# Kernel tuning notes

Measured on AMD Instinct MI355X. Metric: run time of the kernel, lower is better.

Reference implementation:

```python
import jax, jax.numpy as jnp
import numpy as np

T, N, D, V = 512, 256, 1024, 128000  # total tokens, sampled tokens, d_model, vocab


def setup_inputs() -> dict:
    key = jax.random.key(0)
    k1, k2, k3, k4, k5 = jax.random.split(key, 5)
    hidden_states = jax.random.normal(k1, (T, D), dtype=jnp.float32)
    embedding = jax.random.normal(k2, (V, D), dtype=jnp.float32) * 0.02
    # temperatures in [0.5, 1.5): realistic, avoids divide blow-up (0.0 maps to 1.0 in source)
    temperatures = 0.5 + jax.random.uniform(k3, (N,), dtype=jnp.float32)
    # top_p in [0.5, 1.0)
    top_ps = 0.5 + 0.5 * jax.random.uniform(k4, (N,), dtype=jnp.float32)
    last_token_indices = jnp.sort(jax.random.randint(k5, (N,), 0, T))
    return {
        "hidden_states": hidden_states,
        "embedding": embedding,
        "temperatures": temperatures,
        "top_ps": top_ps,
        "last_token_indices": last_token_indices,
    }


def reference(hidden_states, embedding, temperatures, top_ps, last_token_indices):
    # gather last-token hidden states, project to vocab logits
    h = hidden_states[last_token_indices]              # [N, D]
    logits = jnp.einsum("nd,vd->nv", h, embedding)     # [N, V]
    # temperature softmax
    probs = jax.nn.softmax(logits / temperatures[:, None], axis=-1)
    # top-p: descending sort, cumsum, mask tail, renormalize, un-sort
    order = jnp.argsort(-probs, axis=-1)               # descending order indices
    probs_sort = jnp.take_along_axis(probs, order, axis=-1)
    cum = jnp.cumsum(probs_sort, axis=-1)
    mask = (cum - probs_sort) > top_ps[:, None]
    probs_sort = jnp.where(mask, 0.0, probs_sort)
    probs_sort = probs_sort / jnp.sum(probs_sort, axis=-1, keepdims=True)
    inv = jnp.argsort(order, axis=-1)                  # inverse permutation
    probs_f = jnp.take_along_axis(probs_sort, inv, axis=-1)
    # multinomial sampling (one token per row), fixed key for determinism
    tokens = jax.random.categorical(jax.random.key(42), jnp.log(probs_f + 1e-20), axis=-1)
    return probs_f, tokens
```

## Files before the change

kernel.cpp:

```cpp
#include <hip/hip_runtime.h>
#include <stdint.h>

#define N_TOK 256
#define D_MODEL 1024
#define VOCAB 128000
#define NV_ELEMS (256LL * 128000LL)
#define LIST_CAP 24576
#define GLIST_CAP 16384

typedef unsigned long long u64;
typedef uint32_t u32;
typedef __attribute__((ext_vector_type(8))) short bfrag;
typedef __attribute__((ext_vector_type(4))) float facc;

__device__ __forceinline__ uint32_t bf16_rne_bits(float x) {
    uint32_t u = __float_as_uint(x);
    return (u + 0x7fffu + ((u >> 16) & 1u)) >> 16;
}

__device__ __forceinline__ uint32_t rotl32(uint32_t x, int d) {
    return (x << d) | (x >> (32 - d));
}

__device__ __forceinline__ u32 mono32(u32 b) {
    return (b & 0x80000000u) ? ~b : (b | 0x80000000u);
}
__device__ __forceinline__ float unmono32(u32 k) {
    u32 b = (k & 0x80000000u) ? (k & 0x7FFFFFFFu) : ~k;
    return __uint_as_float(b);
}

__device__ __forceinline__ u64 fixmass(float rv) {
    return (u64)(rv * 1073741824.0f);
}

__device__ __forceinline__ uint2 tf_0_42(uint32_t c0, uint32_t c1) {
    const uint32_t ks0 = 0u, ks1 = 42u, ks2 = 0x1BD11BDAu ^ 42u;
    uint32_t x0 = c0 + ks0, x1 = c1 + ks1;
#define R4(a,b,c,d) \
    x0 += x1; x1 = rotl32(x1,a); x1 ^= x0; \
    x0 += x1; x1 = rotl32(x1,b); x1 ^= x0; \
    x0 += x1; x1 = rotl32(x1,c); x1 ^= x0; \
    x0 += x1; x1 = rotl32(x1,d); x1 ^= x0;
    R4(13,15,26,6)   x0 += ks1; x1 += ks2 + 1u;
    R4(17,29,16,24)  x0 += ks2; x1 += ks0 + 2u;
    R4(13,15,26,6)   x0 += ks0; x1 += ks1 + 3u;
    R4(17,29,16,24)  x0 += ks1; x1 += ks2 + 4u;
    R4(13,15,26,6)   x0 += ks2; x1 += ks0 + 5u;
#undef R4
    return make_uint2(x0, x1);
}

__device__ __forceinline__ uint32_t jax_bits(uint32_t j) {
    uint2 r = tf_0_42(0u, j);
    return r.x ^ r.y;
}

__device__ __forceinline__ float jax_gumbel(uint32_t bits) {
    const float TINY = 1.17549435e-38f;
    float u = __uint_as_float((bits >> 9) | 0x3f800000u) - 1.0f;
    u = u + TINY;
    u = fmaxf(TINY, u);
    return -__logf(-__logf(u));
}

__device__ __forceinline__ float rv_of(float l, float rinv) {
    return __expf(l * rinv);
}

__device__ __forceinline__ void async_copy16(const void* g, void* lbase, int lane) {
#if defined(__has_builtin) && __has_builtin(__builtin_amdgcn_global_load_lds)
    __builtin_amdgcn_global_load_lds((const uint32_t*)g, (uint32_t*)lbase, 16, 0, 0);
#else
    *(bfrag*)((char*)lbase + lane * 16) = *(const bfrag*)g;
#endif
}

__device__ __forceinline__ void scan_desc_u64(const u64* h, int nb, u64 carry, u64 P,
                                              int* outCb, u64* outSa) {
    int lane = (int)threadIdx.x & 63;
    int chunk = nb >> 6;
    int top = nb - 1 - lane * chunk;
    u64 ls = 0ull;
    for (int j = 0; j < chunk; ++j) ls += h[top - j];
    u64 incl = ls;
    for (int o = 1; o < 64; o <<= 1) {
        u64 v = __shfl_up(incl, o, 64);
        if (lane >= o) incl += v;
    }
    u64 s0 = carry + incl - ls;
    unsigned long long mask = __ballot(s0 + ls > P);
    if (mask == 0ull) {
        if (lane == 0) { *outCb = 0; *outSa = carry; }
    } else {
        int cstar = (int)__builtin_ctzll(mask);
        if (lane == cstar) {
            u64 sa = s0; int cb = 0;
            for (int j = 0; j < chunk; ++j) {
                int b = top - j;
                if (sa + h[b] > P) { cb = b; break; }
                sa += h[b];
            }
            *outCb = cb; *outSa = sa;
        }
    }
}

__global__ __launch_bounds__(256) void prep_a(
        const float* __restrict__ hidden, const int* __restrict__ idx,
        ushort* __restrict__ wsA) {
    const int m = blockIdx.x;
    const int t = threadIdx.x;
    const float* src = hidden + (long long)idx[m] * D_MODEL;
    const uint32_t swz = (uint32_t)((m & 7) << 4);
    for (int j = 0; j < 4; ++j) {
        int k = t * 4 + j;
        float x = src[k];
        uint32_t hb = bf16_rne_bits(x);
        float hf = __uint_as_float(hb << 16);
        uint32_t lb = bf16_rne_bits(x - hf);
        int kt = k >> 5, kk = k & 31, g = kk >> 3, e = kk & 7;
        char* img = (char*)wsA + (size_t)kt * 32768;
        uint32_t base = (uint32_t)(m * 128 + g * 32);
        *(ushort*)(img + ((base + 0) ^ swz) + e * 2) = (ushort)hb;
        *(ushort*)(img + ((base + 16) ^ swz) + e * 2) = (ushort)lb;
    }
}

__global__ __launch_bounds__(256) void gemm_mfma(
        const ushort* __restrict__ wsA, const float* __restrict__ emb,
        float* __restrict__ logits) {
    __shared__ __align__(16) ushort Aimg[16384];
    __shared__ __align__(16) ushort Bimg[4096];
    const int tid = (int)threadIdx.x;
    const int w = tid >> 6, l = tid & 63;
    const int lr = l & 15, lg = l >> 4;
    const int v0 = blockIdx.x * 64;
    char* Ab = (char*)Aimg;
    char* Bb = (char*)Bimg;

    facc acc[4][4] = {};

    const int rb = tid >> 2, g = tid & 3;
    const float* bbase = emb + (size_t)(v0 + rb) * D_MODEL + g * 8;
    float4 q0 = *(const float4*)(bbase);
    float4 q1 = *(const float4*)(bbase + 4);

    for (int kt = 0; kt < 32; ++kt) {
        __syncthreads();
        const char* asrc = (const char*)wsA + (size_t)kt * 32768;
#pragma unroll
        for (int i = 0; i < 8; ++i) {
            int off = w * 8192 + i * 1024;
            async_copy16(asrc + off + l * 16, Ab + off, l);
        }
        float4 n0 = q0, n1 = q1;
        if (kt < 31) {
            n0 = *(const float4*)(bbase + (kt + 1) * 32);
            n1 = *(const float4*)(bbase + (kt + 1) * 32 + 4);
        }
        {
            float xs[8] = {q0.x, q0.y, q0.z, q0.w, q1.x, q1.y, q1.z, q1.w};
            bfrag h, lo;
#pragma unroll
            for (int e = 0; e < 8; ++e) {
                uint32_t hb = bf16_rne_bits(xs[e]);
                float hf = __uint_as_float(hb << 16);
                uint32_t lb = bf16_rne_bits(xs[e] - hf);
                h[e] = (short)hb; lo[e] = (short)lb;
            }
            uint32_t swz = (uint32_t)((rb & 7) << 4);
            uint32_t base = (uint32_t)(rb * 128 + g * 32);
            *(bfrag*)(Bb + ((base + 0) ^ swz)) = h;
            *(bfrag*)(Bb + ((base + 16) ^ swz)) = lo;
        }
        __syncthreads();
        bfrag bh[4], bl[4];
#pragma unroll
        for (int nj = 0; nj < 4; ++nj) {
            int rbf = nj * 16 + lr;
            uint32_t swz = (uint32_t)((rbf & 7) << 4);
            uint32_t base = (uint32_t)(rbf * 128 + lg * 32);
            bh[nj] = *(const bfrag*)(Bb + ((base + 0) ^ swz));
            bl[nj] = *(const bfrag*)(Bb + ((base + 16) ^ swz));
        }
#pragma unroll
        for (int mi = 0; mi < 4; ++mi) {
            int r = w * 64 + mi * 16 + lr;
            uint32_t swz = (uint32_t)((r & 7) << 4);
            uint32_t base = (uint32_t)(r * 128 + lg * 32);
            bfrag ah = *(const bfrag*)(Ab + ((base + 0) ^ swz));
            bfrag al = *(const bfrag*)(Ab + ((base + 16) ^ swz));
#pragma unroll
            for (int nj = 0; nj < 4; ++nj) {
                acc[mi][nj] = __builtin_amdgcn_mfma_f32_16x16x32_bf16(ah, bh[nj], acc[mi][nj], 0, 0, 0);
                acc[mi][nj] = __builtin_amdgcn_mfma_f32_16x16x32_bf16(ah, bl[nj], acc[mi][nj], 0, 0, 0);
                acc[mi][nj] = __builtin_amdgcn_mfma_f32_16x16x32_bf16(al, bh[nj], acc[mi][nj], 0, 0, 0);
            }
        }
        q0 = n0; q1 = n1;
    }
#pragma unroll
    for (int mi = 0; mi < 4; ++mi) {
        int mbase = w * 64 + mi * 16 + lg * 4;
#pragma unroll
        for (int nj = 0; nj < 4; ++nj) {
            int v = v0 + nj * 16 + lr;
#pragma unroll
            for (int reg = 0; reg < 4; ++reg)
                logits[(size_t)(mbase + reg) * VOCAB + v] = acc[mi][nj][reg];
        }
    }
}

__global__ __launch_bounds__(256) void gemm_kernel(
        const float* __restrict__ hidden, const int* __restrict__ idx,
        const float* __restrict__ emb, float* __restrict__ logits) {
    __shared__ float As[16][64];
    __shared__ float Bs[16][64];
    const int n0 = blockIdx.x * 64, v0 = blockIdx.y * 64;
    const int tid = threadIdx.x;
    const int tx = tid & 15, ty = tid >> 4;
    const int lr = tid >> 2, lk = (tid & 3) * 4;
    float acc[4][4] = {};
    const long long aRow = (long long)idx[n0 + lr] * D_MODEL + lk;
    const long long bRow = (long long)(v0 + lr) * D_MODEL + lk;
    for (int k0 = 0; k0 < D_MODEL; k0 += 16) {
        float4 av = *(const float4*)(hidden + aRow + k0);
        float4 bv = *(const float4*)(emb + bRow + k0);
        __syncthreads();
        As[lk + 0][lr] = av.x; As[lk + 1][lr] = av.y; As[lk + 2][lr] = av.z; As[lk + 3][lr] = av.w;
        Bs[lk + 0][lr] = bv.x; Bs[lk + 1][lr] = bv.y; Bs[lk + 2][lr] = bv.z; Bs[lk + 3][lr] = bv.w;
        __syncthreads();
#pragma unroll
        for (int kk = 0; kk < 16; ++kk) {
            float4 a = *(const float4*)&As[kk][ty * 4];
            float4 b = *(const float4*)&Bs[kk][tx * 4];
            float aa[4] = {a.x, a.y, a.z, a.w};
            float bb[4] = {b.x, b.y, b.z, b.w};
#pragma unroll
            for (int i = 0; i < 4; ++i)
#pragma unroll
                for (int j = 0; j < 4; ++j)
                    acc[i][j] += aa[i] * bb[j];
        }
    }
#pragma unroll
    for (int i = 0; i < 4; ++i) {
        float4 o = make_float4(acc[i][0], acc[i][1], acc[i][2], acc[i][3]);
        *(float4*)(logits + (long long)(n0 + ty * 4 + i) * VOCAB + (v0 + tx * 4)) = o;
    }
}

__global__ __launch_bounds__(512) void hist1_kernel(
        const float* __restrict__ probs, const float* __restrict__ temps,
        u64* __restrict__ ghist) {
    const int row = blockIdx.y, hb = blockIdx.x, tid = (int)threadIdx.x;
    __shared__ u64 h[4096];
    for (int i = tid; i < 4096; i += 512) h[i] = 0ull;
    __syncthreads();
    const float rinv = 1.0f / temps[row];
    const float4* R4 = (const float4*)(probs + (size_t)row * VOCAB);
    const int base4 = hb * 8000;
    for (int i = 0; i < 16; ++i) {
        int j = tid + i * 512;
        if (j < 8000) {
            float4 x = R4[base4 + j];
            float xs[4] = {x.x, x.y, x.z, x.w};
#pragma unroll
            for (int c = 0; c < 4; ++c) {
                u32 key = mono32(__float_as_uint(xs[c]));
                atomicAdd(&h[key >> 20], fixmass(rv_of(xs[c], rinv)));
            }
        }
    }
    __syncthreads();
    u64* gh = ghist + (size_t)row * 4096;
    for (int i = tid; i < 4096; i += 512)
        if (h[i]) atomicAdd(&gh[i], h[i]);
}

__global__ __launch_bounds__(64) void scan1_kernel(
        const u64* __restrict__ ghist, const float* __restrict__ topps,
        u64* __restrict__ rsP, u64* __restrict__ rsCarry, u32* __restrict__ rsCb) {
    const int row = blockIdx.x, lane = (int)threadIdx.x;
    const u64* h = ghist + (size_t)row * 4096;
    u64 S = 0ull;
    for (int j = lane; j < 4096; j += 64) S += h[j];
    for (int o = 32; o >= 1; o >>= 1) S += __shfl_xor(S, o, 64);
    const u64 P = (u64)((double)topps[row] * (double)S);
    __shared__ int sCb; __shared__ u64 sSa;
    scan_desc_u64(h, 4096, 0ull, P, &sCb, &sSa);
    __syncthreads();
    if (lane == 0) { rsP[row] = P; rsCarry[row] = sSa; rsCb[row] = (u32)sCb; }
}

__global__ __launch_bounds__(512) void compact_kernel(
        const float* __restrict__ probs, const u32* __restrict__ rsCb,
        u64* __restrict__ list, u32* __restrict__ listCnt) {
    const int row = blockIdx.y, hb = blockIdx.x, tid = (int)threadIdx.x;
    __shared__ u64 buf[4096];
    __shared__ u32 lcnt, gbase;
    const u32 cb1 = rsCb[row];
    const float4* R4 = (const float4*)(probs + (size_t)row * VOCAB);
    u64* lst = list + (size_t)row * GLIST_CAP;
    const int base4 = hb * 8000;
    if (tid == 0) lcnt = 0u;
    __syncthreads();
    for (int pair = 0; pair < 8; ++pair) {
#pragma unroll
        for (int s = 0; s < 2; ++s) {
            int j = tid + (pair * 2 + s) * 512;
            if (j < 8000) {
                float4 x = R4[base4 + j];
                float xs[4] = {x.x, x.y, x.z, x.w};
#pragma unroll
                for (int c = 0; c < 4; ++c) {
                    u32 key = mono32(__float_as_uint(xs[c]));
                    if ((key >> 20) == cb1) {
                        u32 pos = atomicAdd(&lcnt, 1u);
                        buf[pos] = ((u64)key << 32) | (u32)((base4 + j) * 4 + c);
                    }
                }
            }
        }
        __syncthreads();
        u32 n = lcnt;
        if (n) {
            if (tid == 0) gbase = atomicAdd(&listCnt[row], n);
            __syncthreads();
            u32 gb = gbase;
            for (u32 i2 = tid; i2 < n; i2 += 512) {
                u32 gpos = gb + i2;
                if (gpos < GLIST_CAP) lst[gpos] = buf[i2];
            }
        }
        __syncthreads();
        if (tid == 0) lcnt = 0u;
        __syncthreads();
    }
}

__global__ __launch_bounds__(1024) void resolve_kernel(
        const u64* __restrict__ list, const u32* __restrict__ listCnt,
        const u64* __restrict__ rsP, const u64* __restrict__ rsCarry,
        const u32* __restrict__ rsCb, const float* __restrict__ temps,
        u32* __restrict__ scTs, u32* __restrict__ scTieN,
        float* __restrict__ scInvSp, u32* __restrict__ tieKept) {
    const int row = blockIdx.x, tid = (int)threadIdx.x;
    __shared__ u64 h2[1024];
    __shared__ u32 c3[1024];
    __shared__ int sCb; __shared__ u64 sSa;
    __shared__ u32 sTc;
    __shared__ u32 tlist[1024];
    const u32 cnt = min(listCnt[row], (u32)GLIST_CAP);
    const u64 P = rsP[row];
    const float rinv = 1.0f / temps[row];
    const u64* lst = list + (size_t)row * GLIST_CAP;

    h2[tid] = 0ull;
    __syncthreads();
    for (u32 j = tid; j < cnt; j += 1024) {
        u32 key = (u32)(lst[j] >> 32);
        atomicAdd(&h2[(key >> 10) & 1023u], fixmass(rv_of(unmono32(key), rinv)));
    }
    __syncthreads();
    if (tid < 64) scan_desc_u64(h2, 1024, rsCarry[row], P, &sCb, &sSa);
    __syncthreads();
    const u32 cb2 = (u32)sCb; const u64 carry2 = sSa;
    __syncthreads();

    h2[tid] = 0ull; c3[tid] = 0u;
    __syncthreads();
    for (u32 j = tid; j < cnt; j += 1024) {
        u32 key = (u32)(lst[j] >> 32);
        if (((key >> 10) & 1023u) == cb2) {
            atomicAdd(&h2[key & 1023u], fixmass(rv_of(unmono32(key), rinv)));
            atomicAdd(&c3[key & 1023u], 1u);
        }
    }
    __syncthreads();
    if (tid < 64) scan_desc_u64(h2, 1024, carry2, P, &sCb, &sSa);
    __syncthreads();
    const int cb3 = sCb; const u64 sa3 = sSa;
    const u32 ts = (rsCb[row] << 20) | (cb2 << 10) | (u32)cb3;
    u32 cntb = c3[cb3]; if (cntb == 0u) cntb = 1u;
    const u64 tfq = fixmass(rv_of(unmono32(ts), rinv));
    const u64 rem = P - sa3;
    u32 mt;
    if (tfq == 0ull) mt = cntb;
    else {
        u64 q = rem / tfq;
        mt = (q >= (u64)(cntb - 1)) ? cntb : ((u32)q + 1u);
    }
    const u64 Spq = sa3 + (u64)mt * tfq;

    if (tid == 0) sTc = 0u;
    __syncthreads();
    for (u32 j = tid; j < cnt; j += 1024) {
        if ((u32)(lst[j] >> 32) == ts) {
            u32 pos = atomicAdd(&sTc, 1u);
            if (pos < 1024u) tlist[pos] = (u32)lst[j];
        }
    }
    __syncthreads();
    const u32 tn = min(sTc, 1024u);
    if ((u32)tid < tn) {
        u32 my = tlist[tid];
        u32 rank = 0;
        for (u32 j2 = 0; j2 < tn; ++j2) rank += (tlist[j2] < my) ? 1u : 0u;
        if (rank < mt) tieKept[(size_t)row * 1024 + rank] = my;
    }
    if (tid == 0) {
        scTs[row] = ts;
        scTieN[row] = min(mt, tn);
        scInvSp[row] = (float)(1073741824.0 / (double)Spq);
    }
}

__global__ __launch_bounds__(512) void final2_kernel(
        float* __restrict__ probs, const float* __restrict__ temps,
        const u32* __restrict__ scTs, const u32* __restrict__ scTieN,
        const float* __restrict__ scInvSp, const u32* __restrict__ tieKept,
        u64* __restrict__ argmax) {
    const int row = blockIdx.y, hb = blockIdx.x, tid = (int)threadIdx.x;
    __shared__ u32 tl[1024];
    __shared__ u64 wbest[8];
    const u32 ts = scTs[row], tieN = scTieN[row];
    const float invSp = scInvSp[row];
    const float rinv = 1.0f / temps[row];
    for (u32 i = tid; i < tieN; i += 512) tl[i] = tieKept[(size_t)row * 1024 + i];
    __syncthreads();
    float4* R4 = (float4*)(probs + (size_t)row * VOCAB);
    const u32 rowBase = (u32)row * (u32)VOCAB;
    const int base4 = hb * 8000;
    u64 best = 0ull;
    for (int i = 0; i < 16; ++i) {
        int j = tid + i * 512;
        if (j < 8000) {
            float4 x = R4[base4 + j];
            float xs[4] = {x.x, x.y, x.z, x.w};
            float4 out;
            float* op = (float*)&out;
#pragma unroll
            for (int c = 0; c < 4; ++c) {
                u32 key = mono32(__float_as_uint(xs[c]));
                u32 v = (u32)((base4 + j) * 4 + c);
                bool kept = key > ts;
                if (key == ts) {
                    kept = false;
                    for (u32 q2 = 0; q2 < tieN; ++q2)
                        if (tl[q2] == v) { kept = true; break; }
                }
                if (kept) {
                    float pf = rv_of(xs[c], rinv) * invSp;
                    op[c] = pf;
                    float g = jax_gumbel(jax_bits(rowBase + v));
                    float val = __logf(pf + 1e-20f) + g;
                    u64 pk = ((u64)mono32(__float_as_uint(val)) << 32) | (u32)(~v);
                    if (pk > best) best = pk;
                } else {
                    op[c] = 0.0f;
                }
            }
            R4[base4 + j] = out;
        }
    }
    for (int o = 32; o >= 1; o >>= 1) {
        u64 ob = __shfl_xor(best, o, 64);
        if (ob > best) best = ob;
    }
    if ((tid & 63) == 0) wbest[tid >> 6] = best;
    __syncthreads();
    if (tid == 0) {
        u64 b = wbest[0];
        for (int w2 = 1; w2 < 8; ++w2) if (wbest[w2] > b) b = wbest[w2];
        atomicMax(&argmax[row], b);
    }
}

__global__ void token_kernel(const u64* __restrict__ argmax, float* __restrict__ outTok) {
    int n = (int)threadIdx.x;
    if (n < N_TOK) outTok[n] = (float)(~(u32)argmax[n]);
}

__device__ __forceinline__ void scan_desc_wave(const float* h, int nb, float carry,
                                               float P, int* outCb, float* outSa) {
    int lane = (int)threadIdx.x & 63;
    int chunk = nb >> 6;
    int top = nb - 1 - lane * chunk;
    float ls = 0.0f;
    for (int j = 0; j < chunk; ++j) ls += h[top - j];
    float incl = ls;
    for (int o = 1; o < 64; o <<= 1) {
        float v = __shfl_up(incl, o, 64);
        if (lane >= o) incl += v;
    }
    float s0 = carry + incl - ls;
    unsigned long long mask = __ballot(s0 + ls > P);
    if (mask == 0ull) {
        if (lane == 63) { *outCb = 0; *outSa = carry + incl - h[0]; }
    } else {
        int cstar = (int)__builtin_ctzll(mask);
        if (lane == cstar) {
            float sa = s0; int cb = 0;
            for (int j = 0; j < chunk; ++j) {
                int b = top - j;
                if (sa + h[b] > P) { cb = b; break; }
                sa += h[b];
            }
            *outCb = cb; *outSa = sa;
        }
    }
}

__global__ __launch_bounds__(1024) void sample_kernel(
        float* __restrict__ probs, const float* __restrict__ temps,
        const float* __restrict__ topps, float* __restrict__ outTok) {
    const int row = blockIdx.x;
    const int tid = (int)threadIdx.x;
    float* L = probs + (long long)row * VOCAB;
    const float4* L4 = (const float4*)L;
    float4* L4w = (float4*)L;

    __shared__ float waveH[16][2048];
    __shared__ float hsum[2048];
    __shared__ uint32_t hcnt[1024];
    __shared__ float wred[16];
    __shared__ float aVal[16];
    __shared__ int aIdx[16];
    __shared__ uint32_t tieList[256];
    __shared__ int sCb;
    __shared__ float sSa;
    __shared__ float sP, sCarry1, sCarry2, sSp, sInvSp;
    __shared__ uint32_t sPref1, sCb2, sTsKey, sMt, sTieN, sCnt;
    uint32_t* keys = (uint32_t*)&waveH[4][0];

    const float t = temps[row];
    const float p = topps[row];
    const float rinv = 1.0f / t;

    for (int i = tid; i < 16 * 2048; i += 1024) ((float*)waveH)[i] = 0.0f;
    __syncthreads();
    {
        float* myH = waveH[tid >> 6];
#pragma unroll 2
        for (int i = 0; i < 31; ++i) {
            float4 x = L4[tid + i * 1024];
            float r0 = rv_of(x.x, rinv), r1 = rv_of(x.y, rinv);
            float r2 = rv_of(x.z, rinv), r3 = rv_of(x.w, rinv);
            atomicAdd(&myH[__float_as_uint(r0) >> 20], r0);
            atomicAdd(&myH[__float_as_uint(r1) >> 20], r1);
            atomicAdd(&myH[__float_as_uint(r2) >> 20], r2);
            atomicAdd(&myH[__float_as_uint(r3) >> 20], r3);
        }
        if (tid < 256) {
            float4 x = L4[31744 + tid];
            float r0 = rv_of(x.x, rinv), r1 = rv_of(x.y, rinv);
            float r2 = rv_of(x.z, rinv), r3 = rv_of(x.w, rinv);
            atomicAdd(&myH[__float_as_uint(r0) >> 20], r0);
            atomicAdd(&myH[__float_as_uint(r1) >> 20], r1);
            atomicAdd(&myH[__float_as_uint(r2) >> 20], r2);
            atomicAdd(&myH[__float_as_uint(r3) >> 20], r3);
        }
    }
    __syncthreads();
    {
        float a0 = 0.0f, a1 = 0.0f;
#pragma unroll
        for (int w2 = 0; w2 < 16; ++w2) { a0 += waveH[w2][tid]; a1 += waveH[w2][tid + 1024]; }
        hsum[tid] = a0; hsum[tid + 1024] = a1;
        float s = a0 + a1;
        for (int o = 32; o >= 1; o >>= 1) s += __shfl_xor(s, o, 64);
        if ((tid & 63) == 0) wred[tid >> 6] = s;
    }
    __syncthreads();
    if (tid == 0) {
        float tot = 0.0f;
        for (int w2 = 0; w2 < 16; ++w2) tot += wred[w2];
        sP = p * tot;
    }
    __syncthreads();
    if (tid < 64) scan_desc_wave(hsum, 2048, 0.0f, sP, &sCb, &sSa);
    __syncthreads();
    if (tid == 0) { sPref1 = (uint32_t)sCb; sCarry1 = sSa; sCnt = 0u; }
    __syncthreads();

    const uint32_t pref1 = sPref1;
    const float P = sP;
#pragma unroll 2
    for (int i = 0; i < 31; ++i) {
        float4 x = L4[tid + i * 1024];
        float rr[4] = {rv_of(x.x, rinv), rv_of(x.y, rinv), rv_of(x.z, rinv), rv_of(x.w, rinv)};
#pragma unroll
        for (int c = 0; c < 4; ++c) {
            uint32_t key = __float_as_uint(rr[c]);
            if ((key >> 20) == pref1) {
                uint32_t pos = atomicAdd(&sCnt, 1u);
                if (pos < LIST_CAP) keys[pos] = key;
            }
        }
    }
    if (tid < 256) {
        float4 x = L4[31744 + tid];
        float rr[4] = {rv_of(x.x, rinv), rv_of(x.y, rinv), rv_of(x.z, rinv), rv_of(x.w, rinv)};
#pragma unroll
        for (int c = 0; c < 4; ++c) {
            uint32_t key = __float_as_uint(rr[c]);
            if ((key >> 20) == pref1) {
                uint32_t pos = atomicAdd(&sCnt, 1u);
                if (pos < LIST_CAP) keys[pos] = key;
            }
        }
    }
    __syncthreads();
    const uint32_t K = sCnt;
    const bool inLds = (K <= LIST_CAP);

    if (tid < 1024) hsum[tid] = 0.0f;
    __syncthreads();
    if (inLds) {
        for (uint32_t j = tid; j < K; j += 1024) {
            uint32_t key = keys[j];
            atomicAdd(&hsum[(key >> 10) & 1023u], __uint_as_float(key));
        }
    } else {
        for (int i = 0; i < 125; ++i) {
            int v = tid + i * 1024;
            float rv = rv_of(L[v], rinv);
            uint32_t key = __float_as_uint(rv);
            if ((key >> 20) == pref1) atomicAdd(&hsum[(key >> 10) & 1023u], rv);
        }
    }
    __syncthreads();
    if (tid < 64) scan_desc_wave(hsum, 1024, sCarry1, P, &sCb, &sSa);
    __syncthreads();
    if (tid == 0) { sCb2 = (uint32_t)sCb; sCarry2 = sSa; }
    __syncthreads();

    const uint32_t cb2 = sCb2;
    if (tid < 1024) { hsum[tid] = 0.0f; hcnt[tid] = 0u; }
    __syncthreads();
    if (inLds) {
        for (uint32_t j = tid; j < K; j += 1024) {
            uint32_t key = keys[j];
            if (((key >> 10) & 1023u) == cb2) {
                atomicAdd(&hsum[key & 1023u], __uint_as_float(key));
                atomicAdd(&hcnt[key & 1023u], 1u);
            }
        }
    } else {
        const uint32_t pref2full = (pref1 << 10) | cb2;
        for (int i = 0; i < 125; ++i) {
            int v = tid + i * 1024;
            float rv = rv_of(L[v], rinv);
            uint32_t key = __float_as_uint(rv);
            if ((key >> 10) == pref2full) {
                atomicAdd(&hsum[key & 1023u], rv);
                atomicAdd(&hcnt[key & 1023u], 1u);
            }
        }
    }
    __syncthreads();
    if (tid < 64) scan_desc_wave(hsum, 1024, sCarry2, P, &sCb, &sSa);
    __syncthreads();
    if (tid == 0) {
        int cb3 = sCb; float sa3 = sSa;
        uint32_t ts = (pref1 << 20) | (cb2 << 10) | (uint32_t)cb3;
        uint32_t cnt = hcnt[cb3]; if (cnt == 0u) cnt = 1u;
        float tf = __uint_as_float(ts);
        uint32_t mt;
        float rem = P - sa3; if (rem < 0.0f) rem = 0.0f;
        if (!(tf > 0.0f)) mt = cnt;
        else {
            float q = floorf(rem / tf);
            mt = (q >= (float)(cnt - 1)) ? cnt : ((uint32_t)q + 1u);
        }
        sTsKey = ts; sMt = mt;
        sSp = sa3 + (float)mt * tf;
        sInvSp = 1.0f / sSp;
        sTieN = 0u;
    }
    __syncthreads();

    const uint32_t ts = sTsKey, mt = sMt;
    const float invSp = sInvSp;
    float bestV = -INFINITY;
    int bestI = 0x7FFFFFFF;
    const uint32_t rowBase = (uint32_t)row * (uint32_t)VOCAB;
    for (int i = 0; i < 32; ++i) {
        int f4i = (i < 31) ? (tid + i * 1024) : (31744 + tid);
        if (i == 31 && tid >= 256) break;
        float4 x = L4[f4i];
        float rr[4] = {rv_of(x.x, rinv), rv_of(x.y, rinv), rv_of(x.z, rinv), rv_of(x.w, rinv)};
        float4 out;
        float* op = (float*)&out;
#pragma unroll
        for (int c = 0; c < 4; ++c) {
            uint32_t key = __float_as_uint(rr[c]);
            int v = f4i * 4 + c;
            if (key > ts) {
                float pf = rr[c] * invSp;
                op[c] = pf;
                float g = jax_gumbel(jax_bits(rowBase + (uint32_t)v));
                float val = __logf(pf + 1e-20f) + g;
                if (val > bestV || (val == bestV && v < bestI)) { bestV = val; bestI = v; }
            } else if (key == ts) {
                op[c] = 0.0f;
                uint32_t pos = atomicAdd(&sTieN, 1u);
                if (pos < 256u) tieList[pos] = (uint32_t)v;
            } else {
                op[c] = 0.0f;
            }
        }
        L4w[f4i] = out;
    }
    __syncthreads();
    {
        const uint32_t tn = min(sTieN, 256u);
        if ((uint32_t)tid < tn) {
            uint32_t v = tieList[tid];
            uint32_t rank = 0;
            for (uint32_t j = 0; j < tn; ++j) rank += (tieList[j] < v) ? 1u : 0u;
            if (rank < mt) {
                float pf = __uint_as_float(ts) * invSp;
                L[v] = pf;
                float g = jax_gumbel(jax_bits(rowBase + v));
                float val = __logf(pf + 1e-20f) + g;
                if (val > bestV || (val == bestV && (int)v < bestI)) { bestV = val; bestI = (int)v; }
            }
        }
    }
    for (int o = 32; o >= 1; o >>= 1) {
        float ov = __shfl_xor(bestV, o, 64);
        int oi = __shfl_xor(bestI, o, 64);
        if (ov > bestV || (ov == bestV && oi < bestI)) { bestV = ov; bestI = oi; }
    }
    if ((tid & 63) == 0) { aVal[tid >> 6] = bestV; aIdx[tid >> 6] = bestI; }
    __syncthreads();
    if (tid == 0) {
        float bv = aVal[0]; int bi = aIdx[0];
        for (int w2 = 1; w2 < 16; ++w2) {
            if (aVal[w2] > bv || (aVal[w2] == bv && aIdx[w2] < bi)) { bv = aVal[w2]; bi = aIdx[w2]; }
        }
        outTok[row] = (float)bi;
    }
}

extern "C" void kernel_launch(void* const* d_in, const int* in_sizes, int n_in,
                              void* d_out, int out_size, void* d_ws, size_t ws_size,
                              hipStream_t stream) {
    const float* hidden = (const float*)d_in[0];
    const float* emb    = (const float*)d_in[1];
    const float* temps  = (const float*)d_in[2];
    const float* topps  = (const float*)d_in[3];
    const int*   idx    = (const int*)d_in[4];

    float* probs  = (float*)d_out;
    float* outTok = probs + NV_ELEMS;

    char* ws = (char*)d_ws;
    const bool wsGemm = ws_size >= (size_t)(1u << 20);
    const bool wsBig  = ws_size >= (size_t)(44u << 20);

    if (wsBig) {
        u64* ghist   = (u64*)(ws + (1u << 20));
        char* m      = ws + (41u << 20);
        hipMemsetAsync(ghist, 0, (size_t)256 * 4096 * 8, stream);
        hipMemsetAsync(m, 0, 1024, stream);
        hipMemsetAsync(m + 9216, 0, 2048, stream);
    }

    if (wsGemm) {
        ushort* wsA = (ushort*)ws;
        prep_a<<<N_TOK, 256, 0, stream>>>(hidden, idx, wsA);
        gemm_mfma<<<VOCAB / 64, 256, 0, stream>>>(wsA, emb, probs);
    } else {
        gemm_kernel<<<dim3(4, 2000), 256, 0, stream>>>(hidden, idx, emb, probs);
    }

    if (wsBig) {
        u64* ghist     = (u64*)(ws + (1u << 20));
        u64* list      = (u64*)(ws + (9u << 20));
        char* m        = ws + (41u << 20);
        u32* listCnt   = (u32*)(m);
        u32* rsCb      = (u32*)(m + 1024);
        u64* rsP       = (u64*)(m + 2048);
        u64* rsCarry   = (u64*)(m + 4096);
        u32* scTs      = (u32*)(m + 6144);
        u32* scTieN    = (u32*)(m + 7168);
        float* scInvSp = (float*)(m + 8192);
        u64* argmax    = (u64*)(m + 9216);
        u32* tieKept   = (u32*)(m + 16384);

        hist1_kernel<<<dim3(4, N_TOK), 512, 0, stream>>>(probs, temps, ghist);
        scan1_kernel<<<N_TOK, 64, 0, stream>>>(ghist, topps, rsP, rsCarry, rsCb);
        compact_kernel<<<dim3(4, N_TOK), 512, 0, stream>>>(probs, rsCb, list, listCnt);
        resolve_kernel<<<N_TOK, 1024, 0, stream>>>(list, listCnt, rsP, rsCarry, rsCb,
                                                   temps, scTs, scTieN, scInvSp, tieKept);
        final2_kernel<<<dim3(4, N_TOK), 512, 0, stream>>>(probs, temps, scTs, scTieN,
                                                          scInvSp, tieKept, argmax);
        token_kernel<<<1, 256, 0, stream>>>(argmax, outTok);
    } else {
        sample_kernel<<<N_TOK, 1024, 0, stream>>>(probs, temps, topps, outTok);
    }
}
```

Baseline: 501.0 us.

## Double-buffer GEMM LDS tiles and replace histogram atomics with per-block partials

```diff
diff --git a/kernel.cpp b/kernel.cpp
--- a/kernel.cpp
+++ b/kernel.cpp
@@ -127,54 +127,66 @@
     }
 }
 
+__device__ __forceinline__ void bconv_write(char* Bb, float4 x0, float4 x1,
+                                            int rb, int g) {
+    float xs[8] = {x0.x, x0.y, x0.z, x0.w, x1.x, x1.y, x1.z, x1.w};
+    bfrag h, lo;
+#pragma unroll
+    for (int e = 0; e < 8; ++e) {
+        uint32_t hb = bf16_rne_bits(xs[e]);
+        float hf = __uint_as_float(hb << 16);
+        uint32_t lb = bf16_rne_bits(xs[e] - hf);
+        h[e] = (short)hb; lo[e] = (short)lb;
+    }
+    uint32_t swz = (uint32_t)((rb & 7) << 4);
+    uint32_t base = (uint32_t)(rb * 128 + g * 32);
+    *(bfrag*)(Bb + ((base + 0) ^ swz)) = h;
+    *(bfrag*)(Bb + ((base + 16) ^ swz)) = lo;
+}
+
 __global__ __launch_bounds__(256) void gemm_mfma(
         const ushort* __restrict__ wsA, const float* __restrict__ emb,
         float* __restrict__ logits) {
-    __shared__ __align__(16) ushort Aimg[16384];
-    __shared__ __align__(16) ushort Bimg[4096];
+    __shared__ __align__(16) ushort Aimg[2][16384];
+    __shared__ __align__(16) ushort Bimg[2][4096];
     const int tid = (int)threadIdx.x;
     const int w = tid >> 6, l = tid & 63;
     const int lr = l & 15, lg = l >> 4;
     const int v0 = blockIdx.x * 64;
-    char* Ab = (char*)Aimg;
-    char* Bb = (char*)Bimg;
 
     facc acc[4][4] = {};
 
     const int rb = tid >> 2, g = tid & 3;
     const float* bbase = emb + (size_t)(v0 + rb) * D_MODEL + g * 8;
-    float4 q0 = *(const float4*)(bbase);
-    float4 q1 = *(const float4*)(bbase + 4);
-
-    for (int kt = 0; kt < 32; ++kt) {
-        __syncthreads();
-        const char* asrc = (const char*)wsA + (size_t)kt * 32768;
+
+    {
+        const char* asrc = (const char*)wsA;
 #pragma unroll
         for (int i = 0; i < 8; ++i) {
             int off = w * 8192 + i * 1024;
-            async_copy16(asrc + off + l * 16, Ab + off, l);
-        }
-        float4 n0 = q0, n1 = q1;
+            async_copy16(asrc + off + l * 16, (char*)Aimg[0] + off, l);
+        }
+        float4 x0 = *(const float4*)(bbase);
+        float4 x1 = *(const float4*)(bbase + 4);
+        bconv_write((char*)Bimg[0], x0, x1, rb, g);
+    }
+    __syncthreads();
+
+    for (int kt = 0; kt < 32; ++kt) {
+        const int cur = kt & 1, nxt = cur ^ 1;
+        float4 n0 = {}, n1 = {};
         if (kt < 31) {
+            const char* asrc = (const char*)wsA + (size_t)(kt + 1) * 32768;
+#pragma unroll
+            for (int i = 0; i < 8; ++i) {
+                int off = w * 8192 + i * 1024;
+                async_copy16(asrc + off + l * 16, (char*)Aimg[nxt] + off, l);
+            }
             n0 = *(const float4*)(bbase + (kt + 1) * 32);
             n1 = *(const float4*)(bbase + (kt + 1) * 32 + 4);
         }
-        {
-            float xs[8] = {q0.x, q0.y, q0.z, q0.w, q1.x, q1.y, q1.z, q1.w};
-            bfrag h, lo;
-#pragma unroll
-            for (int e = 0; e < 8; ++e) {
-                uint32_t hb = bf16_rne_bits(xs[e]);
-                float hf = __uint_as_float(hb << 16);
-                uint32_t lb = bf16_rne_bits(xs[e] - hf);
-                h[e] = (short)hb; lo[e] = (short)lb;
-            }
-            uint32_t swz = (uint32_t)((rb & 7) << 4);
-            uint32_t base = (uint32_t)(rb * 128 + g * 32);
-            *(bfrag*)(Bb + ((base + 0) ^ swz)) = h;
-            *(bfrag*)(Bb + ((base + 16) ^ swz)) = lo;
-        }
-        __syncthreads();
+        char* Ab = (char*)Aimg[cur];
+        char* Bb = (char*)Bimg[cur];
         bfrag bh[4], bl[4];
 #pragma unroll
         for (int nj = 0; nj < 4; ++nj) {
@@ -198,7 +210,8 @@
                 acc[mi][nj] = __builtin_amdgcn_mfma_f32_16x16x32_bf16(al, bh[nj], acc[mi][nj], 0, 0, 0);
             }
         }
-        q0 = n0; q1 = n1;
+        if (kt < 31) bconv_write((char*)Bimg[nxt], n0, n1, rb, g);
+        __syncthreads();
     }
 #pragma unroll
     for (int mi = 0; mi < 4; ++mi) {
@@ -254,7 +267,7 @@
 
 __global__ __launch_bounds__(512) void hist1_kernel(
         const float* __restrict__ probs, const float* __restrict__ temps,
-        u64* __restrict__ ghist) {
+        u64* __restrict__ hpart) {
     const int row = blockIdx.y, hb = blockIdx.x, tid = (int)threadIdx.x;
     __shared__ u64 h[4096];
     for (int i = tid; i < 4096; i += 512) h[i] = 0ull;
@@ -275,24 +288,33 @@
         }
     }
     __syncthreads();
-    u64* gh = ghist + (size_t)row * 4096;
-    for (int i = tid; i < 4096; i += 512)
-        if (h[i]) atomicAdd(&gh[i], h[i]);
+    u64* gh = hpart + ((size_t)row * 4 + hb) * 4096;
+    for (int i = tid; i < 4096; i += 512) gh[i] = h[i];
 }
 
 __global__ __launch_bounds__(64) void scan1_kernel(
-        const u64* __restrict__ ghist, const float* __restrict__ topps,
-        u64* __restrict__ rsP, u64* __restrict__ rsCarry, u32* __restrict__ rsCb) {
+        const u64* __restrict__ hpart, const float* __restrict__ topps,
+        u64* __restrict__ rsP, u64* __restrict__ rsCarry, u32* __restrict__ rsCb,
+        u32* __restrict__ listCnt, u64* __restrict__ argmax) {
     const int row = blockIdx.x, lane = (int)threadIdx.x;
-    const u64* h = ghist + (size_t)row * 4096;
+    __shared__ u64 sh[4096];
+    const u64* hp = hpart + (size_t)row * 4 * 4096;
     u64 S = 0ull;
-    for (int j = lane; j < 4096; j += 64) S += h[j];
+    for (int j = lane; j < 4096; j += 64) {
+        u64 v = hp[j] + hp[4096 + j] + hp[8192 + j] + hp[12288 + j];
+        sh[j] = v;
+        S += v;
+    }
+    __syncthreads();
     for (int o = 32; o >= 1; o >>= 1) S += __shfl_xor(S, o, 64);
     const u64 P = (u64)((double)topps[row] * (double)S);
     __shared__ int sCb; __shared__ u64 sSa;
-    scan_desc_u64(h, 4096, 0ull, P, &sCb, &sSa);
-    __syncthreads();
-    if (lane == 0) { rsP[row] = P; rsCarry[row] = sSa; rsCb[row] = (u32)sCb; }
+    scan_desc_u64(sh, 4096, 0ull, P, &sCb, &sSa);
+    __syncthreads();
+    if (lane == 0) {
+        rsP[row] = P; rsCarry[row] = sSa; rsCb[row] = (u32)sCb;
+        listCnt[row] = 0u; argmax[row] = 0ull;
+    }
 }
 
 __global__ __launch_bounds__(512) void compact_kernel(
@@ -763,14 +785,6 @@
     const bool wsGemm = ws_size >= (size_t)(1u << 20);
     const bool wsBig  = ws_size >= (size_t)(44u << 20);
 
-    if (wsBig) {
-        u64* ghist   = (u64*)(ws + (1u << 20));
-        char* m      = ws + (41u << 20);
-        hipMemsetAsync(ghist, 0, (size_t)256 * 4096 * 8, stream);
-        hipMemsetAsync(m, 0, 1024, stream);
-        hipMemsetAsync(m + 9216, 0, 2048, stream);
-    }
-
     if (wsGemm) {
         ushort* wsA = (ushort*)ws;
         prep_a<<<N_TOK, 256, 0, stream>>>(hidden, idx, wsA);
@@ -780,7 +794,6 @@
     }
 
     if (wsBig) {
-        u64* ghist     = (u64*)(ws + (1u << 20));
         u64* list      = (u64*)(ws + (9u << 20));
         char* m        = ws + (41u << 20);
         u32* listCnt   = (u32*)(m);
@@ -793,8 +806,9 @@
         u64* argmax    = (u64*)(m + 9216);
         u32* tieKept   = (u32*)(m + 16384);
 
-        hist1_kernel<<<dim3(4, N_TOK), 512, 0, stream>>>(probs, temps, ghist);
-        scan1_kernel<<<N_TOK, 64, 0, stream>>>(ghist, topps, rsP, rsCarry, rsCb);
+        hist1_kernel<<<dim3(4, N_TOK), 512, 0, stream>>>(probs, temps, list);
+        scan1_kernel<<<N_TOK, 64, 0, stream>>>(list, topps, rsP, rsCarry, rsCb,
+                                               listCnt, argmax);
         compact_kernel<<<dim3(4, N_TOK), 512, 0, stream>>>(probs, rsCb, list, listCnt);
         resolve_kernel<<<N_TOK, 1024, 0, stream>>>(list, listCnt, rsP, rsCarry, rsCb,
                                                    temps, scTs, scTieN, scInvSp, tieKept);
```

Measured after the change: 488.4 us. 2.5% less time.
